# Optimization experiments

Measured on AMD Instinct MI355X. Metric: run time of the kernel, lower is better.

## Reference

```python
import jax, jax.numpy as jnp
import numpy as np

NQ = 8    # QCNN qubits
NLQ = 4   # QLSTM qubits == hidden_dim
C64 = jnp.complex64

H_GATE = (1.0 / np.sqrt(2.0)) * jnp.array([[1, 1], [1, -1]], dtype=C64)


def ap1(st, U, q):
    # apply 2x2 gate U on qubit axis q of state st (shape (2,)*n)
    s = jnp.moveaxis(st, q, -1)
    s = jnp.einsum('ij,...j->...i', U, s)
    return jnp.moveaxis(s, -1, q)


def apcx(st, c, t):
    # CNOT with control c, target t: flip target slice where control == 1
    s = jnp.moveaxis(st, (c, t), (-2, -1))
    s = jnp.stack([s[..., 0, :], s[..., 1, ::-1]], axis=-2)
    return jnp.moveaxis(s, (-2, -1), (c, t))


def RX(t):
    c = jnp.cos(t / 2).astype(C64)
    s = (-1j * jnp.sin(t / 2)).astype(C64)
    return jnp.stack([jnp.stack([c, s]), jnp.stack([s, c])])


def RY(t):
    c = jnp.cos(t / 2)
    s = jnp.sin(t / 2)
    return jnp.stack([jnp.stack([c, -s]), jnp.stack([s, c])]).astype(C64)


def RZ(t):
    e = jnp.exp(-0.5j * t).astype(C64)
    z = jnp.zeros((), C64)
    return jnp.stack([jnp.stack([e, z]), jnp.stack([z, jnp.conj(e)])])


def PH(t):
    # qiskit phase gate P(t) = diag(1, e^{i t})
    e = jnp.exp(1j * t).astype(C64)
    o = jnp.ones((), C64)
    z = jnp.zeros((), C64)
    return jnp.stack([jnp.stack([o, z]), jnp.stack([z, e])])


def init_state(n):
    st = jnp.zeros((2,) * n, C64)
    return st.at[(0,) * n].set(1.0)


def zexp(st, q):
    # <Z_q> of statevector st
    p = st.real ** 2 + st.imag ** 2
    m = p.sum(axis=tuple(a for a in range(st.ndim) if a != q))
    return m[0] - m[1]


def conv_block(st, p, q1, q2):
    st = ap1(st, RZ(-np.pi / 2), q2)
    st = apcx(st, q2, q1)
    st = ap1(st, RZ(p[0]), q1)
    st = ap1(st, RY(p[1]), q2)
    st = apcx(st, q1, q2)
    st = ap1(st, RY(p[2]), q2)
    st = apcx(st, q2, q1)
    st = ap1(st, RZ(np.pi / 2), q1)
    return st


def pool_block(st, p, src, sink):
    st = ap1(st, RZ(-np.pi / 2), sink)
    st = apcx(st, sink, src)
    st = ap1(st, RZ(p[0]), src)
    st = ap1(st, RY(p[1]), sink)
    st = apcx(st, src, sink)
    st = ap1(st, RY(p[2]), sink)
    return st


QCNN_SPECS = [
    (conv_block, [(0, 1), (2, 3), (4, 5), (6, 7)]),  # c1
    (pool_block, [(0, 1), (2, 3), (4, 5), (6, 7)]),  # p1
    (conv_block, [(0, 1), (2, 3)]),                  # c2
    (pool_block, [(0, 1), (2, 3)]),                  # p2
    (conv_block, [(0, 1)]),                          # c3
    (pool_block, [(0, 1)]),                          # p3
]


def qcnn_single(x, w):
    # x: (8,) feature angles, w: (42,) ansatz weights
    st = init_state(NQ)
    for _ in range(2):
        for q in range(NQ):
            st = ap1(st, H_GATE, q)
        for q in range(NQ):
            st = ap1(st, PH(2.0 * x[q]), q)
    idx = 0
    for blk, prs in QCNN_SPECS:
        for a, b in prs:
            st = blk(st, w[idx:idx + 3], a, b)
            idx += 3
    return zexp(st, NQ - 1)  # 'ZIIIIIII' => Z on qubit 7 (little-endian)


def qgate_single(v, theta):
    # v: (4,) encoder angles (per sample), theta: (4,) trainable RX angles
    st = init_state(NLQ)
    for i in range(NLQ):
        st = ap1(st, RX(v[i]), i)
    for i in range(NLQ):
        st = ap1(st, RX(theta[i]), i)
    for i in range(NLQ - 1):
        st = apcx(st, i, i + 1)
    st = apcx(st, NLQ - 1, 0)
    return jnp.stack([zexp(st, q) for q in range(NLQ)])


qgate = jax.vmap(qgate_single, in_axes=(0, None))


def setup_inputs() -> dict:
    key = jax.random.key(0)
    ks = jax.random.split(key, 12)
    B, S = 16, 128
    x = jax.random.uniform(ks[0], (B, S, NQ), jnp.float32) * np.pi
    qcnn_w = jax.random.normal(ks[1], (42,), jnp.float32) * 0.1

    def lin(k, out_d, in_d):
        k1, k2 = jax.random.split(k)
        lim = 1.0 / np.sqrt(in_d)
        W = jax.random.uniform(k1, (out_d, in_d), jnp.float32, -lim, lim)
        b = jax.random.uniform(k2, (out_d,), jnp.float32, -lim, lim)
        return W, b

    Wf, bf = lin(ks[2], NLQ, 1 + NLQ)
    Wi, bi = lin(ks[3], NLQ, 1 + NLQ)
    Wg, bg = lin(ks[4], NLQ, 1 + NLQ)
    Wo, bo = lin(ks[5], NLQ, 1 + NLQ)
    theta_f = jax.random.normal(ks[6], (NLQ,), jnp.float32) * 0.1
    theta_i = jax.random.normal(ks[7], (NLQ,), jnp.float32) * 0.1
    theta_g = jax.random.normal(ks[8], (NLQ,), jnp.float32) * 0.1
    theta_o = jax.random.normal(ks[9], (NLQ,), jnp.float32) * 0.1
    Wh, bh = lin(ks[10], 1, NLQ)
    return dict(x=x, qcnn_w=qcnn_w, theta_f=theta_f, theta_i=theta_i,
                theta_g=theta_g, theta_o=theta_o, Wf=Wf, bf=bf, Wi=Wi, bi=bi,
                Wg=Wg, bg=bg, Wo=Wo, bo=bo, Wh=Wh, bh=bh)


def reference(x, qcnn_w, theta_f, theta_i, theta_g, theta_o,
              Wf, bf, Wi, bi, Wg, bg, Wo, bo, Wh, bh):
    B, S, _ = x.shape
    flat = x.reshape(B * S, NQ)
    qcnn_out = jax.vmap(qcnn_single, in_axes=(0, None))(flat, qcnn_w)
    qcnn_out = qcnn_out.reshape(B, S, 1)
    lstm_in = jnp.transpose(qcnn_out, (1, 0, 2))  # (S, B, 1)
    h0 = jnp.zeros((B, NLQ), x.dtype)
    c0 = jnp.zeros((B, NLQ), x.dtype)

    def step(carry, xt):
        hx, cx = carry
        comb = jnp.concatenate([xt, hx], axis=1)  # (B, 1 + hidden)
        f = jax.nn.sigmoid(qgate(comb @ Wf.T + bf, theta_f))
        i = jax.nn.sigmoid(qgate(comb @ Wi.T + bi, theta_i))
        g = jnp.tanh(qgate(comb @ Wg.T + bg, theta_g))
        o = jax.nn.sigmoid(qgate(comb @ Wo.T + bo, theta_o))
        cx = f * cx + i * g
        hx = o * jnp.tanh(cx)
        return (hx, cx), hx

    _, outs = jax.lax.scan(step, (h0, c0), lstm_in)  # outs: (S, B, hidden)
    logits = outs[-1] @ Wh.T + bh  # (B, 1)
    return qcnn_out, logits
```

## Files before the change

kernel.cpp:

```cpp
#include <hip/hip_runtime.h>
#include <math.h>

#define PI_F 3.14159265358979323846f

__device__ __forceinline__ float rcpf(float x) { return __builtin_amdgcn_rcpf(x); }
__device__ __forceinline__ void fswap(float2& p, float2& q) { float2 t = p; p = q; q = t; }


template<int Q>
__device__ __forceinline__ float exq(float v) {
    if constexpr (Q == 2)
        return __int_as_float(__builtin_amdgcn_update_dpp(0, __float_as_int(v), 0xB1, 0xF, 0xF, true));
    else if constexpr (Q == 3)
        return __int_as_float(__builtin_amdgcn_update_dpp(0, __float_as_int(v), 0x4E, 0xF, 0xF, true));
    else if constexpr (Q == 4)
        return __int_as_float(__builtin_amdgcn_ds_swizzle(__float_as_int(v), 0x101F));
    else if constexpr (Q == 5)
        return __int_as_float(__builtin_amdgcn_ds_swizzle(__float_as_int(v), 0x201F));
    else if constexpr (Q == 6)
        return __int_as_float(__builtin_amdgcn_ds_swizzle(__float_as_int(v), 0x401F));
    else
        return __shfl_xor(v, 32, 64);
}

template<int Q>
__device__ __forceinline__ void rzg(float2 a[4], float th, int lane) {
    float c = __cosf(0.5f * th), s = __sinf(0.5f * th);
    if constexpr (Q >= 2) {
        float se = ((lane >> (Q - 2)) & 1) ? s : -s;
        #pragma unroll
        for (int r = 0; r < 4; ++r) {
            float nx = c * a[r].x - se * a[r].y;
            float ny = c * a[r].y + se * a[r].x;
            a[r] = make_float2(nx, ny);
        }
    } else {
        #pragma unroll
        for (int r = 0; r < 4; ++r) {
            int bit = (Q == 0) ? (r >> 1) : (r & 1);
            float se = bit ? s : -s;
            float nx = c * a[r].x - se * a[r].y;
            float ny = c * a[r].y + se * a[r].x;
            a[r] = make_float2(nx, ny);
        }
    }
}

template<int Q>
__device__ __forceinline__ void ryg(float2 a[4], float th, int lane) {
    float c = __cosf(0.5f * th), s = __sinf(0.5f * th);
    if constexpr (Q >= 2) {
        float se = ((lane >> (Q - 2)) & 1) ? s : -s;
        #pragma unroll
        for (int r = 0; r < 4; ++r) {
            float ox = exq<Q>(a[r].x), oy = exq<Q>(a[r].y);
            a[r] = make_float2(c * a[r].x + se * ox, c * a[r].y + se * oy);
        }
    } else if constexpr (Q == 0) {
        #pragma unroll
        for (int r = 0; r < 2; ++r) {
            float2 lo = a[r], hi = a[r + 2];
            a[r]     = make_float2(c * lo.x - s * hi.x, c * lo.y - s * hi.y);
            a[r + 2] = make_float2(s * lo.x + c * hi.x, s * lo.y + c * hi.y);
        }
    } else {
        #pragma unroll
        for (int r = 0; r < 4; r += 2) {
            float2 lo = a[r], hi = a[r + 1];
            a[r]     = make_float2(c * lo.x - s * hi.x, c * lo.y - s * hi.y);
            a[r + 1] = make_float2(s * lo.x + c * hi.x, s * lo.y + c * hi.y);
        }
    }
}

template<int C, int T>
__device__ __forceinline__ void cxg(float2 a[4], int lane) {
    if constexpr (C >= 2) {
        bool cb = (lane >> (C - 2)) & 1;
        #pragma unroll
        for (int r = 0; r < 4; ++r) {
            float ox = exq<T>(a[r].x), oy = exq<T>(a[r].y);
            a[r].x = cb ? ox : a[r].x;
            a[r].y = cb ? oy : a[r].y;
        }
    } else if constexpr (C == 0 && T == 1) {
        fswap(a[2], a[3]);
    } else {
        fswap(a[1], a[3]);
    }
}

template<int Q>
__device__ __forceinline__ void featg(float2 a[4], float xq, int lane) {
    float phi = 2.0f * xq;
    float e1x = __cosf(phi), e1y = __sinf(phi);
    float e2x = e1x * e1x - e1y * e1y;
    float e2y = 2.0f * e1x * e1y;
    float2 u00 = make_float2(0.5f * (1.0f + e1x),  0.5f * e1y);
    float2 u01 = make_float2(0.5f * (1.0f - e1x), -0.5f * e1y);
    float2 u10 = make_float2(0.5f * (e1x - e2x), 0.5f * (e1y - e2y));
    float2 u11 = make_float2(0.5f * (e1x + e2x), 0.5f * (e1y + e2y));
    if constexpr (Q >= 2) {
        bool bset = (lane >> (Q - 2)) & 1;
        float csx = bset ? u11.x : u00.x, csy = bset ? u11.y : u00.y;
        float cox = bset ? u10.x : u01.x, coy = bset ? u10.y : u01.y;
        #pragma unroll
        for (int r = 0; r < 4; ++r) {
            float ox = exq<Q>(a[r].x), oy = exq<Q>(a[r].y);
            float nx = csx * a[r].x - csy * a[r].y + cox * ox - coy * oy;
            float ny = csx * a[r].y + csy * a[r].x + cox * oy + coy * ox;
            a[r] = make_float2(nx, ny);
        }
    } else {
        float2 l, h;
        #define APPL(LO, HI)                                                        \
            l = a[LO]; h = a[HI];                                                   \
            a[LO] = make_float2(u00.x*l.x - u00.y*l.y + u01.x*h.x - u01.y*h.y,      \
                                u00.x*l.y + u00.y*l.x + u01.x*h.y + u01.y*h.x);     \
            a[HI] = make_float2(u10.x*l.x - u10.y*l.y + u11.x*h.x - u11.y*h.y,      \
                                u10.x*l.y + u10.y*l.x + u11.x*h.y + u11.y*h.x);
        if constexpr (Q == 0) { APPL(0, 2) APPL(1, 3) }
        else                  { APPL(0, 1) APPL(2, 3) }
        #undef APPL
    }
}

template<int Q1, int Q2>
__device__ __forceinline__ void convg(float2 a[4], const float* __restrict__ p, int lane) {
    rzg<Q2>(a, -0.5f * PI_F, lane);
    cxg<Q2, Q1>(a, lane);
    rzg<Q1>(a, p[0], lane);
    ryg<Q2>(a, p[1], lane);
    cxg<Q1, Q2>(a, lane);
    ryg<Q2>(a, p[2], lane);
    cxg<Q2, Q1>(a, lane);
    rzg<Q1>(a, 0.5f * PI_F, lane);
}

template<int Q1, int Q2>
__device__ __forceinline__ void poolg(float2 a[4], const float* __restrict__ p, int lane) {
    rzg<Q2>(a, -0.5f * PI_F, lane);
    cxg<Q2, Q1>(a, lane);
    rzg<Q1>(a, p[0], lane);
    ryg<Q2>(a, p[1], lane);
    cxg<Q1, Q2>(a, lane);
    ryg<Q2>(a, p[2], lane);
}

__global__ __launch_bounds__(64) void qcnn_kernel(const float* __restrict__ x,
                                                  const float* __restrict__ w,
                                                  float* __restrict__ out) {
    int n = blockIdx.x;
    int lane = threadIdx.x;
    float2 a[4];
    a[0] = make_float2(lane == 0 ? 1.0f : 0.0f, 0.0f);
    a[1] = make_float2(0.0f, 0.0f);
    a[2] = make_float2(0.0f, 0.0f);
    a[3] = make_float2(0.0f, 0.0f);

    const float* xr = x + n * 8;
    featg<0>(a, xr[0], lane);
    featg<1>(a, xr[1], lane);
    featg<2>(a, xr[2], lane);
    featg<3>(a, xr[3], lane);
    featg<4>(a, xr[4], lane);
    featg<5>(a, xr[5], lane);
    featg<6>(a, xr[6], lane);
    featg<7>(a, xr[7], lane);

    convg<0,1>(a, w + 0,  lane);
    convg<2,3>(a, w + 3,  lane);
    convg<4,5>(a, w + 6,  lane);
    convg<6,7>(a, w + 9,  lane);
    poolg<0,1>(a, w + 12, lane);
    poolg<2,3>(a, w + 15, lane);
    poolg<4,5>(a, w + 18, lane);
    poolg<6,7>(a, w + 21, lane);
    convg<0,1>(a, w + 24, lane);
    convg<2,3>(a, w + 27, lane);
    poolg<0,1>(a, w + 30, lane);
    poolg<2,3>(a, w + 33, lane);
    convg<0,1>(a, w + 36, lane);
    poolg<0,1>(a, w + 39, lane);

    float ssum = 0.f;
    #pragma unroll
    for (int r = 0; r < 4; ++r)
        ssum += a[r].x * a[r].x + a[r].y * a[r].y;
    ssum = (lane & 32) ? -ssum : ssum;
    #pragma unroll
    for (int m = 1; m < 64; m <<= 1)
        ssum += __shfl_xor(ssum, m, 64);
    if (lane == 0) out[n] = ssum;
}


template<int CTRL>
__device__ __forceinline__ float bq(float v) {
    return __int_as_float(__builtin_amdgcn_update_dpp(0, __float_as_int(v), CTRL, 0xF, 0xF, true));
}

__global__ __launch_bounds__(64) void qlstm_kernel(
    const float* __restrict__ qc,
    const float* __restrict__ thf, const float* __restrict__ thi,
    const float* __restrict__ thg, const float* __restrict__ tho,
    const float* __restrict__ Wf, const float* __restrict__ bf,
    const float* __restrict__ Wi, const float* __restrict__ bi,
    const float* __restrict__ Wg, const float* __restrict__ bg,
    const float* __restrict__ Wo, const float* __restrict__ bo,
    const float* __restrict__ Wh, const float* __restrict__ bh,
    float* __restrict__ out) {
    __shared__ __align__(16) float qsh[16 * 132];
    int lane = threadIdx.x;

    const float4* qc4 = (const float4*)qc;
    #pragma unroll
    for (int k = 0; k < 8; ++k) {
        int i = k * 64 + lane;
        float4 v = qc4[i];
        int b = i >> 5;
        int t = (i & 31) << 2;
        *(float4*)&qsh[b * 132 + t] = v;
    }
    __builtin_amdgcn_wave_barrier();

    int b = lane >> 2, g = lane & 3;
    const float* Wp = (g == 0) ? Wf : (g == 1) ? Wi : (g == 2) ? Wg : Wo;
    const float* bp = (g == 0) ? bf : (g == 1) ? bi : (g == 2) ? bg : bo;
    const float* tp = (g == 0) ? thf : (g == 1) ? thi : (g == 2) ? thg : tho;

    float W[20], av[4];
    #pragma unroll
    for (int k = 0; k < 20; ++k) W[k] = Wp[k];
    #pragma unroll
    for (int r = 0; r < 4; ++r) av[r] = bp[r] + tp[r];

    bool isG = (g == 2);
    float es = isG ? 2.0f : -1.0f;

    float c0 = 0.f, c1 = 0.f, c2 = 0.f, c3 = 0.f;
    float h0 = 0.f, h1 = 0.f, h2 = 0.f, h3 = 0.f;
    const float* qrow = &qsh[b * 132];

    for (int t = 0; t < 128; ++t) {
        float xv = qrow[t];
        float vA = av[0] + W[0]*xv  + W[1]*h0  + W[2]*h1  + W[3]*h2  + W[4]*h3;
        float vB = av[1] + W[5]*xv  + W[6]*h0  + W[7]*h1  + W[8]*h2  + W[9]*h3;
        float vC = av[2] + W[10]*xv + W[11]*h0 + W[12]*h1 + W[13]*h2 + W[14]*h3;
        float vD = av[3] + W[15]*xv + W[16]*h0 + W[17]*h1 + W[18]*h2 + W[19]*h3;
        float cA = __cosf(vA), cB = __cosf(vB), cC = __cosf(vC), cD = __cosf(vD);
        float rB = cA * cB, rC = rB * cC, rD = rC * cD, rA = cB * (cC * cD);
        float EA = __expf(es * rA), EB = __expf(es * rB);
        float EC = __expf(es * rC), ED = __expf(es * rD);
        float nA = (isG ? EA - 1.0f : 1.0f) * rcpf(EA + 1.0f);
        float nB = (isG ? EB - 1.0f : 1.0f) * rcpf(EB + 1.0f);
        float nC = (isG ? EC - 1.0f : 1.0f) * rcpf(EC + 1.0f);
        float nD = (isG ? ED - 1.0f : 1.0f) * rcpf(ED + 1.0f);
        float FA = bq<0x00>(nA), IA = bq<0x55>(nA), GA = bq<0xAA>(nA), OA = bq<0xFF>(nA);
        float FB = bq<0x00>(nB), IB = bq<0x55>(nB), GB = bq<0xAA>(nB), OB = bq<0xFF>(nB);
        float FC = bq<0x00>(nC), IC = bq<0x55>(nC), GC = bq<0xAA>(nC), OC = bq<0xFF>(nC);
        float FD = bq<0x00>(nD), ID = bq<0x55>(nD), GD = bq<0xAA>(nD), OD = bq<0xFF>(nD);
        c0 = FA * c0 + IA * GA;
        c1 = FB * c1 + IB * GB;
        c2 = FC * c2 + IC * GC;
        c3 = FD * c3 + ID * GD;
        float E0 = __expf(2.0f * c0), E1 = __expf(2.0f * c1);
        float E2 = __expf(2.0f * c2), E3 = __expf(2.0f * c3);
        h0 = OA * (E0 - 1.0f) * rcpf(E0 + 1.0f);
        h1 = OB * (E1 - 1.0f) * rcpf(E1 + 1.0f);
        h2 = OC * (E2 - 1.0f) * rcpf(E2 + 1.0f);
        h3 = OD * (E3 - 1.0f) * rcpf(E3 + 1.0f);
    }

    if (g == 0)
        out[2048 + b] = bh[0] + Wh[0]*h0 + Wh[1]*h1 + Wh[2]*h2 + Wh[3]*h3;
}

extern "C" void kernel_launch(void* const* d_in, const int* in_sizes, int n_in,
                              void* d_out, int out_size, void* d_ws, size_t ws_size,
                              hipStream_t stream) {
    const float* x = (const float*)d_in[0];
    const float* w = (const float*)d_in[1];
    float* out = (float*)d_out;

    qcnn_kernel<<<2048, 64, 0, stream>>>(x, w, out);
    qlstm_kernel<<<1, 64, 0, stream>>>(
        out,
        (const float*)d_in[2], (const float*)d_in[3],
        (const float*)d_in[4], (const float*)d_in[5],
        (const float*)d_in[6], (const float*)d_in[7],
        (const float*)d_in[8], (const float*)d_in[9],
        (const float*)d_in[10], (const float*)d_in[11],
        (const float*)d_in[12], (const float*)d_in[13],
        (const float*)d_in[14], (const float*)d_in[15],
        out);
}
```

Baseline: 127.0 us.

## Pack four circuits per QCNN block and split LSTM cell update across lanes

The QCNN kernel now launches 512 blocks of 256 threads, with four circuits per block instead of one 64-thread block each, to cut per-block scheduling overhead. In the QLSTM recurrence, each lane now keeps one cell state instead of four redundant copies. It picks its F/I/G/O gate values with selects, computes one tanh, and broadcasts h back through DPP. The gate nonlinearity is rewritten as an affine of a single reciprocal, and the next timestep's input is prefetched from LDS. This shortens the serial dependency chain per step, at the cost of extra DPP broadcasts and selects.

```diff
diff --git a/kernel.cpp b/kernel.cpp
--- a/kernel.cpp
+++ b/kernel.cpp
@@ -147,11 +147,11 @@
     ryg<Q2>(a, p[2], lane);
 }
 
-__global__ __launch_bounds__(64) void qcnn_kernel(const float* __restrict__ x,
-                                                  const float* __restrict__ w,
-                                                  float* __restrict__ out) {
-    int n = blockIdx.x;
-    int lane = threadIdx.x;
+__global__ __launch_bounds__(256) void qcnn_kernel(const float* __restrict__ x,
+                                                   const float* __restrict__ w,
+                                                   float* __restrict__ out) {
+    int lane = threadIdx.x & 63;
+    int n = blockIdx.x * 4 + (threadIdx.x >> 6);
     float2 a[4];
     a[0] = make_float2(lane == 0 ? 1.0f : 0.0f, 0.0f);
     a[1] = make_float2(0.0f, 0.0f);
@@ -200,6 +200,12 @@
     return __int_as_float(__builtin_amdgcn_update_dpp(0, __float_as_int(v), CTRL, 0xF, 0xF, true));
 }
 
+__device__ __forceinline__ float pick4(bool b0, bool b1, float a0, float a1, float a2, float a3) {
+    float t01 = b0 ? a1 : a0;
+    float t23 = b0 ? a3 : a2;
+    return b1 ? t23 : t01;
+}
+
 __global__ __launch_bounds__(64) void qlstm_kernel(
     const float* __restrict__ qc,
     const float* __restrict__ thf, const float* __restrict__ thi,
@@ -224,10 +230,11 @@
     }
     __builtin_amdgcn_wave_barrier();
 
-    int b = lane >> 2, g = lane & 3;
-    const float* Wp = (g == 0) ? Wf : (g == 1) ? Wi : (g == 2) ? Wg : Wo;
-    const float* bp = (g == 0) ? bf : (g == 1) ? bi : (g == 2) ? bg : bo;
-    const float* tp = (g == 0) ? thf : (g == 1) ? thi : (g == 2) ? thg : tho;
+    int b = lane >> 2, q = lane & 3;
+    bool qb0 = q & 1, qb1 = q & 2;
+    const float* Wp = (q == 0) ? Wf : (q == 1) ? Wi : (q == 2) ? Wg : Wo;
+    const float* bp = (q == 0) ? bf : (q == 1) ? bi : (q == 2) ? bg : bo;
+    const float* tp = (q == 0) ? thf : (q == 1) ? thi : (q == 2) ? thg : tho;
 
     float W[20], av[4];
     #pragma unroll
@@ -235,44 +242,49 @@
     #pragma unroll
     for (int r = 0; r < 4; ++r) av[r] = bp[r] + tp[r];
 
-    bool isG = (g == 2);
-    float es = isG ? 2.0f : -1.0f;
-
-    float c0 = 0.f, c1 = 0.f, c2 = 0.f, c3 = 0.f;
+    float nA = (q == 2) ? 1.0f : 0.0f;
+    float nB = (q == 2) ? -2.0f : 1.0f;
+    float nK = (q == 2) ? 2.0f : -1.0f;
+
+    float c = 0.f;
     float h0 = 0.f, h1 = 0.f, h2 = 0.f, h3 = 0.f;
     const float* qrow = &qsh[b * 132];
+    float xv = qrow[0];
 
     for (int t = 0; t < 128; ++t) {
-        float xv = qrow[t];
+        float xn = qrow[t + 1];
         float vA = av[0] + W[0]*xv  + W[1]*h0  + W[2]*h1  + W[3]*h2  + W[4]*h3;
         float vB = av[1] + W[5]*xv  + W[6]*h0  + W[7]*h1  + W[8]*h2  + W[9]*h3;
         float vC = av[2] + W[10]*xv + W[11]*h0 + W[12]*h1 + W[13]*h2 + W[14]*h3;
         float vD = av[3] + W[15]*xv + W[16]*h0 + W[17]*h1 + W[18]*h2 + W[19]*h3;
         float cA = __cosf(vA), cB = __cosf(vB), cC = __cosf(vC), cD = __cosf(vD);
-        float rB = cA * cB, rC = rB * cC, rD = rC * cD, rA = cB * (cC * cD);
-        float EA = __expf(es * rA), EB = __expf(es * rB);
-        float EC = __expf(es * rC), ED = __expf(es * rD);
-        float nA = (isG ? EA - 1.0f : 1.0f) * rcpf(EA + 1.0f);
-        float nB = (isG ? EB - 1.0f : 1.0f) * rcpf(EB + 1.0f);
-        float nC = (isG ? EC - 1.0f : 1.0f) * rcpf(EC + 1.0f);
-        float nD = (isG ? ED - 1.0f : 1.0f) * rcpf(ED + 1.0f);
-        float FA = bq<0x00>(nA), IA = bq<0x55>(nA), GA = bq<0xAA>(nA), OA = bq<0xFF>(nA);
-        float FB = bq<0x00>(nB), IB = bq<0x55>(nB), GB = bq<0xAA>(nB), OB = bq<0xFF>(nB);
-        float FC = bq<0x00>(nC), IC = bq<0x55>(nC), GC = bq<0xAA>(nC), OC = bq<0xFF>(nC);
-        float FD = bq<0x00>(nD), ID = bq<0x55>(nD), GD = bq<0xAA>(nD), OD = bq<0xFF>(nD);
-        c0 = FA * c0 + IA * GA;
-        c1 = FB * c1 + IB * GB;
-        c2 = FC * c2 + IC * GC;
-        c3 = FD * c3 + ID * GD;
-        float E0 = __expf(2.0f * c0), E1 = __expf(2.0f * c1);
-        float E2 = __expf(2.0f * c2), E3 = __expf(2.0f * c3);
-        h0 = OA * (E0 - 1.0f) * rcpf(E0 + 1.0f);
-        h1 = OB * (E1 - 1.0f) * rcpf(E1 + 1.0f);
-        h2 = OC * (E2 - 1.0f) * rcpf(E2 + 1.0f);
-        h3 = OD * (E3 - 1.0f) * rcpf(E3 + 1.0f);
-    }
-
-    if (g == 0)
+        float r1 = cA * cB, r2 = r1 * cC, r3 = r2 * cD, r0 = cB * (cC * cD);
+        float E0 = __expf(nK * r0), E1 = __expf(nK * r1);
+        float E2 = __expf(nK * r2), E3 = __expf(nK * r3);
+        float n0 = nA + nB * rcpf(E0 + 1.0f);
+        float n1 = nA + nB * rcpf(E1 + 1.0f);
+        float n2 = nA + nB * rcpf(E2 + 1.0f);
+        float n3 = nA + nB * rcpf(E3 + 1.0f);
+        float F0 = bq<0x00>(n0), F1 = bq<0x00>(n1), F2 = bq<0x00>(n2), F3 = bq<0x00>(n3);
+        float I0 = bq<0x55>(n0), I1 = bq<0x55>(n1), I2 = bq<0x55>(n2), I3 = bq<0x55>(n3);
+        float G0 = bq<0xAA>(n0), G1 = bq<0xAA>(n1), G2 = bq<0xAA>(n2), G3 = bq<0xAA>(n3);
+        float O0 = bq<0xFF>(n0), O1 = bq<0xFF>(n1), O2 = bq<0xFF>(n2), O3 = bq<0xFF>(n3);
+        float F = pick4(qb0, qb1, F0, F1, F2, F3);
+        float I = pick4(qb0, qb1, I0, I1, I2, I3);
+        float G = pick4(qb0, qb1, G0, G1, G2, G3);
+        float O = pick4(qb0, qb1, O0, O1, O2, O3);
+        c = F * c + I * G;
+        float Ec = __expf(2.0f * c);
+        float tau = 1.0f - 2.0f * rcpf(Ec + 1.0f);
+        float hq = O * tau;
+        h0 = bq<0x00>(hq);
+        h1 = bq<0x55>(hq);
+        h2 = bq<0xAA>(hq);
+        h3 = bq<0xFF>(hq);
+        xv = xn;
+    }
+
+    if (q == 0)
         out[2048 + b] = bh[0] + Wh[0]*h0 + Wh[1]*h1 + Wh[2]*h2 + Wh[3]*h3;
 }
 
@@ -283,7 +295,7 @@
     const float* w = (const float*)d_in[1];
     float* out = (float*)d_out;
 
-    qcnn_kernel<<<2048, 64, 0, stream>>>(x, w, out);
+    qcnn_kernel<<<512, 256, 0, stream>>>(x, w, out);
     qlstm_kernel<<<1, 64, 0, stream>>>(
         out,
         (const float*)d_in[2], (const float*)d_in[3],
```

After: 122.5 us. -3.6%, faster.
